# Optimization experiments

Hardware: AMD Instinct MI355X
Metric: run time of the kernel (lower is better)

Reference implementation:

```python
import jax, jax.numpy as jnp
from jax import lax
import numpy as np

HID = 64
NL = 4

def conv2d(x, w, b):
    # x: (N,C,H,W), w: (O,I,kh,kw)
    y = lax.conv_general_dilated(x, w, (1, 1), 'SAME',
                                 dimension_numbers=('NCHW', 'OIHW', 'NCHW'))
    return y + b[None, :, None, None]


def stlstm_cell(x, h, c, m, Wx, bx, Wh, bh, Wm, bm, Wo, bo, Wl, bl):
    # standard PredRNN SpatioTemporalLSTM cell
    xc = conv2d(x, Wx, bx)            # 7*HID channels
    hc = conv2d(h, Wh, bh)            # 4*HID
    mc = conv2d(m, Wm, bm)            # 3*HID
    ix, fx, gx, ixp, fxp, gxp, ox = jnp.split(xc, 7, axis=1)
    ih, fh, gh, oh = jnp.split(hc, 4, axis=1)
    im, fm, gm = jnp.split(mc, 3, axis=1)
    i_t = jax.nn.sigmoid(ix + ih)
    f_t = jax.nn.sigmoid(fx + fh)
    g_t = jnp.tanh(gx + gh)
    c_new = f_t * c + i_t * g_t
    i_tp = jax.nn.sigmoid(ixp + im)
    f_tp = jax.nn.sigmoid(fxp + fm)
    g_tp = jnp.tanh(gxp + gm)
    m_new = f_tp * m + i_tp * g_tp
    mem = jnp.concatenate([c_new, m_new], axis=1)  # 2*HID
    o_t = jax.nn.sigmoid(ox + oh + conv2d(mem, Wo, bo))
    h_new = o_t * jnp.tanh(conv2d(mem, Wl, bl))
    return h_new, c_new, m_new


def setup_inputs() -> dict:
    key = jax.random.key(0)
    ks = jax.random.split(key, 16)
    B, L, C, H, W = 8, 10, 1, 256, 256
    x = jax.random.normal(ks[0], (B, L, C, H, W), dtype=jnp.float32)
    s = 0.02
    d = dict(
        x=x, in_len=10, out_len=10,
        Wx=jax.random.normal(ks[1], (NL, 7 * HID, HID, 3, 3), jnp.float32) * s,
        bx=jnp.zeros((NL, 7 * HID), jnp.float32),
        Wh=jax.random.normal(ks[2], (NL, 4 * HID, HID, 3, 3), jnp.float32) * s,
        bh=jnp.zeros((NL, 4 * HID), jnp.float32),
        Wm=jax.random.normal(ks[3], (NL, 3 * HID, HID, 3, 3), jnp.float32) * s,
        bm=jnp.zeros((NL, 3 * HID), jnp.float32),
        Wo=jax.random.normal(ks[4], (NL, HID, 2 * HID, 3, 3), jnp.float32) * s,
        bo=jnp.zeros((NL, HID), jnp.float32),
        Wl=jax.random.normal(ks[5], (NL, HID, 2 * HID, 1, 1), jnp.float32) * s,
        bl=jnp.zeros((NL, HID), jnp.float32),
        Wd=jax.random.normal(ks[6], (64, HID, 3, 3), jnp.float32) * s,
        bd=jnp.zeros((64,), jnp.float32),
    )
    return d


def reference(x, in_len, out_len, Wx, bx, Wh, bh, Wm, bm, Wo, bo, Wl, bl, Wd, bd):
    B, L, C, H, W = x.shape
    ph, pw = H // 8, W // 8
    # patch_division: space-to-depth 8x8
    xp = x.reshape(B, L, C, 8, ph, 8, pw).transpose(0, 1, 2, 3, 5, 4, 6)
    xp = xp.reshape(B, L, C * 64, ph, pw)
    T = in_len + out_len - 1  # 19 steps
    pad = jnp.zeros((B, T - in_len, C * 64, ph, pw), xp.dtype)
    xs_seq = jnp.moveaxis(jnp.concatenate([xp, pad], axis=1), 1, 0)  # (T,B,64,ph,pw)
    flags = jnp.arange(T) < in_len
    z = jnp.zeros((NL, B, HID, ph, pw), xp.dtype)
    carry0 = (z, z, jnp.zeros((B, HID, ph, pw), xp.dtype),
              jnp.zeros((B, HID, ph, pw), xp.dtype))

    def step(carry, inp):
        hs, cs, m, htop = carry
        xt, flag = inp
        cur = jnp.where(flag, xt, htop)
        new_h, new_c = [], []
        for l in range(NL):
            h, c, m = stlstm_cell(cur, hs[l], cs[l], m,
                                  Wx[l], bx[l], Wh[l], bh[l], Wm[l], bm[l],
                                  Wo[l], bo[l], Wl[l], bl[l])
            new_h.append(h)
            new_c.append(c)
            cur = h
        return (jnp.stack(new_h), jnp.stack(new_c), m, cur), cur

    _, outs = lax.scan(step, carry0, (xs_seq, flags))  # (T,B,HID,ph,pw)
    y = jnp.moveaxis(outs, 0, 1).reshape(B * T, HID, ph, pw)
    y = jax.nn.sigmoid(conv2d(y, Wd, bd)).reshape(B, T, 64, ph, pw)
    # patch_combination: depth-to-space 8x8
    out = y.reshape(B, T, 1, 8, 8, ph, pw).transpose(0, 1, 2, 3, 5, 4, 6)
    out = out.reshape(B, T, 1, 8 * ph, 8 * pw)
    return out
```

## Files before the change

kernel.cpp:

```cpp
#include <hip/hip_runtime.h>
#include <hip/hip_bf16.h>


typedef __bf16 bf16x8 __attribute__((ext_vector_type(8)));
typedef float f32x4 __attribute__((ext_vector_type(4)));

namespace {
constexpr int  T     = 19;
constexpr int  INLEN = 10;

constexpr long OFF_XPB   = 0;
constexpr long OFF_OUTSB = 2621440;
constexpr long OFF_HB    = 7602176;
constexpr long OFF_MB    = 8650752;
constexpr long OFF_C     = 9175040;
constexpr long OFF_M     = 11272192;
constexpr long OFF_MEMB  = 11796480;
constexpr long OFF_OP    = 12320768;
constexpr long OFF_WFA   = 12845056;
constexpr long OFF_WFB   = 13877248;
constexpr long OFF_WFD   = 14041088;
constexpr long OFF_BA    = 14059520;
constexpr long WS_NEEDED_FLOATS = 14061312;
}

__device__ __forceinline__ float sigf(float x)     { return 1.f / (1.f + __expf(-x)); }
__device__ __forceinline__ float tanhfast(float x) { return 2.f / (1.f + __expf(-2.f * x)) - 1.f; }
__device__ __forceinline__ unsigned short f2b(float f) {
  __hip_bfloat16 h = __float2bfloat16(f);
  return __builtin_bit_cast(unsigned short, h);
}
__device__ __forceinline__ f32x4 mfma16(bf16x8 a, bf16x8 b, f32x4 c) {
  return __builtin_amdgcn_mfma_f32_16x16x32_bf16(a, b, c, 0, 0, 0);
}

__global__ __launch_bounds__(448) void kcellA(
    const unsigned short* __restrict__ in0, long in0bs,
    const unsigned short* __restrict__ hB,
    const unsigned short* __restrict__ mBr,
    const unsigned short* __restrict__ wfA,
    const float* __restrict__ bA,
    float* __restrict__ C, float* __restrict__ M,
    unsigned short* __restrict__ mBw,
    unsigned short* __restrict__ memB,
    float* __restrict__ op)
{
  __shared__ __align__(16) char smem[57344];
  unsigned short* sIn = (unsigned short*)smem;
  float* sEx = (float*)smem;

  const int b = blockIdx.x, r0 = blockIdx.y, tid = threadIdx.x;
  const unsigned short* base0 = in0 + (long)b * in0bs;
  const unsigned short* base1 = hB  + (long)b * 65536;
  const unsigned short* base2 = mBr + (long)b * 65536;

  for (int s = tid; s < 3 * 816; s += 448) {
    int inp = s / 816, rem = s - inp * 816;
    int slot = rem >> 3, cg = rem & 7;
    int rr = slot / 34, cl = slot - rr * 34;
    int gr = r0 - 1 + rr, gc = cl - 1;
    const unsigned short* bp = (inp == 0) ? base0 : ((inp == 1) ? base1 : base2);
    uint4 v = make_uint4(0u, 0u, 0u, 0u);
    if ((unsigned)gr < 32u && (unsigned)gc < 32u)
      v = *(const uint4*)(bp + ((long)(gr * 32 + gc) << 6) + cg * 8);
    *(uint4*)(sIn + inp * 6528 + slot * 64 + ((cg ^ (slot & 7)) * 8)) = v;
  }
  __syncthreads();

  const int w = tid >> 6, lane = tid & 63, q = lane >> 4, n16 = lane & 15;
  f32x4 acc[4][2];
  #pragma unroll
  for (int i = 0; i < 4; ++i) { acc[i][0] = (f32x4){0,0,0,0}; acc[i][1] = (f32x4){0,0,0,0}; }

  const unsigned short* sb1 = sIn + ((w < 4) ? 6528 : 13056);
  const unsigned short* wbase = wfA + (long)w * 73728;

  #pragma unroll
  for (int p = 0; p < 2; ++p) {
    const unsigned short* sb = p ? sb1 : sIn;
    #pragma unroll
    for (int tap = 0; tap < 9; ++tap) {
      const int dy = tap / 3, dx = tap - dy * 3;
      #pragma unroll
      for (int cc = 0; cc < 2; ++cc) {
        const unsigned short* wp = wbase + (long)(((p * 9 + tap) * 2 + cc) * 4) * 512 + lane * 8;
        bf16x8 a0 = *(const bf16x8*)(wp);
        bf16x8 a1 = *(const bf16x8*)(wp + 512);
        bf16x8 a2 = *(const bf16x8*)(wp + 1024);
        bf16x8 a3 = *(const bf16x8*)(wp + 1536);
        const int g = cc * 4 + q;
        bf16x8 bf0, bf1;
        { int slot = dy * 34 + n16 + dx;
          bf0 = *(const bf16x8*)(sb + slot * 64 + ((g ^ (slot & 7)) * 8)); }
        { int slot = dy * 34 + 16 + n16 + dx;
          bf1 = *(const bf16x8*)(sb + slot * 64 + ((g ^ (slot & 7)) * 8)); }
        acc[0][0] = mfma16(a0, bf0, acc[0][0]); acc[0][1] = mfma16(a0, bf1, acc[0][1]);
        acc[1][0] = mfma16(a1, bf0, acc[1][0]); acc[1][1] = mfma16(a1, bf1, acc[1][1]);
        acc[2][0] = mfma16(a2, bf0, acc[2][0]); acc[2][1] = mfma16(a2, bf1, acc[2][1]);
        acc[3][0] = mfma16(a3, bf0, acc[3][0]); acc[3][1] = mfma16(a3, bf1, acc[3][1]);
      }
    }
  }

  __syncthreads();
  #pragma unroll
  for (int i = 0; i < 4; ++i)
    #pragma unroll
    for (int j = 0; j < 2; ++j)
      #pragma unroll
      for (int r = 0; r < 4; ++r)
        sEx[w * 2048 + (i * 16 + q * 4 + r) * 32 + (j * 16 + n16)] = acc[i][j][r];
  __syncthreads();

  for (int idx = tid; idx < 2048; idx += 448) {
    const int ch = idx >> 5, pxl = idx & 31;
    const int pxg = r0 * 32 + pxl;
    float iv = sEx[idx]            + bA[ch];
    float fv = sEx[2048 + idx]     + bA[64 + ch];
    float gv = sEx[4096 + idx]     + bA[128 + ch];
    float ov = sEx[6144 + idx]     + bA[192 + ch];
    float i2 = sEx[8192 + idx]     + bA[256 + ch];
    float f2 = sEx[10240 + idx]    + bA[320 + ch];
    float g2 = sEx[12288 + idx]    + bA[384 + ch];
    const long cmo = ((long)b * 64 + ch) * 1024 + pxg;
    float cn = sigf(fv) * C[cmo] + sigf(iv) * tanhfast(gv);
    float mn = sigf(f2) * M[cmo] + sigf(i2) * tanhfast(g2);
    C[cmo] = cn; M[cmo] = mn; op[cmo] = ov;
    const long mo = (long)b * 1024 + pxg;
    memB[mo * 128 + ch]      = f2b(cn);
    memB[mo * 128 + 64 + ch] = f2b(mn);
    mBw[mo * 64 + ch]        = f2b(mn);
  }
}

__global__ __launch_bounds__(512) void kcellB(
    const unsigned short* __restrict__ memB,
    const unsigned short* __restrict__ wfB,
    const float* __restrict__ op, const float* __restrict__ bl,
    unsigned short* __restrict__ hBw, unsigned short* __restrict__ outsBt,
    int writeOuts)
{
  __shared__ __align__(16) char smem[73728];
  unsigned short* sIn = (unsigned short*)smem;
  float* sEx = (float*)smem;

  const int b = blockIdx.x, r0 = blockIdx.y, tid = threadIdx.x;
  const unsigned short* bp = memB + (long)b * 131072;
  for (int s = tid; s < 102 * 16; s += 512) {
    int slot = s >> 4, cg = s & 15;
    int rr = slot / 34, cl = slot - rr * 34;
    int gr = r0 - 1 + rr, gc = cl - 1;
    uint4 v = make_uint4(0u, 0u, 0u, 0u);
    if ((unsigned)gr < 32u && (unsigned)gc < 32u)
      v = *(const uint4*)(bp + ((long)(gr * 32 + gc) << 7) + cg * 8);
    *(uint4*)(sIn + slot * 128 + ((cg ^ (slot & 7)) * 8)) = v;
  }
  __syncthreads();

  const int w = tid >> 6, lane = tid & 63, q = lane >> 4, n16 = lane & 15;
  f32x4 accO[4][2], accL[4][2];
  #pragma unroll
  for (int i = 0; i < 4; ++i) {
    accO[i][0] = (f32x4){0,0,0,0}; accO[i][1] = (f32x4){0,0,0,0};
    accL[i][0] = (f32x4){0,0,0,0}; accL[i][1] = (f32x4){0,0,0,0};
  }

  #pragma unroll
  for (int s5 = 0; s5 < 5; ++s5) {
    const int s = w * 5 + s5;
    const bool isL = (s >= 36);
    const int tap = isL ? 4 : (s >> 2);
    const int cc  = isL ? (s - 36) : (s & 3);
    const int dy = tap / 3, dx = tap - dy * 3;
    const unsigned short* wp = wfB + (long)s * 2048 + lane * 8;
    bf16x8 a0 = *(const bf16x8*)(wp);
    bf16x8 a1 = *(const bf16x8*)(wp + 512);
    bf16x8 a2 = *(const bf16x8*)(wp + 1024);
    bf16x8 a3 = *(const bf16x8*)(wp + 1536);
    const int g = cc * 4 + q;
    bf16x8 bf0, bf1;
    { int slot = dy * 34 + n16 + dx;
      bf0 = *(const bf16x8*)(sIn + slot * 128 + ((g ^ (slot & 7)) * 8)); }
    { int slot = dy * 34 + 16 + n16 + dx;
      bf1 = *(const bf16x8*)(sIn + slot * 128 + ((g ^ (slot & 7)) * 8)); }
    if (isL) {
      accL[0][0] = mfma16(a0, bf0, accL[0][0]); accL[0][1] = mfma16(a0, bf1, accL[0][1]);
      accL[1][0] = mfma16(a1, bf0, accL[1][0]); accL[1][1] = mfma16(a1, bf1, accL[1][1]);
      accL[2][0] = mfma16(a2, bf0, accL[2][0]); accL[2][1] = mfma16(a2, bf1, accL[2][1]);
      accL[3][0] = mfma16(a3, bf0, accL[3][0]); accL[3][1] = mfma16(a3, bf1, accL[3][1]);
    } else {
      accO[0][0] = mfma16(a0, bf0, accO[0][0]); accO[0][1] = mfma16(a0, bf1, accO[0][1]);
      accO[1][0] = mfma16(a1, bf0, accO[1][0]); accO[1][1] = mfma16(a1, bf1, accO[1][1]);
      accO[2][0] = mfma16(a2, bf0, accO[2][0]); accO[2][1] = mfma16(a2, bf1, accO[2][1]);
      accO[3][0] = mfma16(a3, bf0, accO[3][0]); accO[3][1] = mfma16(a3, bf1, accO[3][1]);
    }
  }

  __syncthreads();
  #pragma unroll
  for (int i = 0; i < 4; ++i)
    #pragma unroll
    for (int j = 0; j < 2; ++j)
      #pragma unroll
      for (int r = 0; r < 4; ++r)
        sEx[w * 2048 + (i * 16 + q * 4 + r) * 32 + (j * 16 + n16)] = accO[i][j][r];
  if (w == 7) {
    #pragma unroll
    for (int i = 0; i < 4; ++i)
      #pragma unroll
      for (int j = 0; j < 2; ++j)
        #pragma unroll
        for (int r = 0; r < 4; ++r)
          sEx[16384 + (i * 16 + q * 4 + r) * 32 + (j * 16 + n16)] = accL[i][j][r];
  }
  __syncthreads();

  for (int idx = tid; idx < 2048; idx += 512) {
    const int ch = idx >> 5, pxl = idx & 31;
    const int pxg = r0 * 32 + pxl;
    float o = op[((long)b * 64 + ch) * 1024 + pxg];
    #pragma unroll
    for (int ww = 0; ww < 8; ++ww) o += sEx[ww * 2048 + idx];
    float l = sEx[16384 + idx] + bl[ch];
    unsigned short hv = f2b(sigf(o) * tanhfast(l));
    hBw[((long)b * 1024 + pxg) * 64 + ch] = hv;
    if (writeOuts) outsBt[((long)b * 1024 + pxg) * 64 + ch] = hv;
  }
}

__device__ __forceinline__ void conv3_acc(
    const unsigned short* __restrict__ ip, int ciStride, int ciOff,
    const unsigned short* __restrict__ wf, int ncc, int ccoff,
    unsigned short* sIn, f32x4 (&acc)[4][4])
{
  const int tid = threadIdx.x;
  const int r0  = (int)blockIdx.y * 8;
  for (int s = tid; s < 2720; s += 256) {
    int slot = s >> 3, cg = s & 7;
    int rr = slot / 34, cl = slot - rr * 34;
    int gr = r0 - 1 + rr, gc = cl - 1;
    uint4 v = make_uint4(0u, 0u, 0u, 0u);
    if ((unsigned)gr < 32u && (unsigned)gc < 32u)
      v = *(const uint4*)(ip + (long)(gr * 32 + gc) * ciStride + ciOff + cg * 8);
    *(uint4*)(sIn + slot * 64 + ((cg ^ (slot & 7)) * 8)) = v;
  }
  __syncthreads();
  const int lane = tid & 63, w = tid >> 6;
  const int q = lane >> 4, n16 = lane & 15;
  #pragma unroll
  for (int i = 0; i < 4; ++i)
    #pragma unroll
    for (int j = 0; j < 4; ++j)
      acc[i][j] = (f32x4){0.f, 0.f, 0.f, 0.f};
  #pragma unroll
  for (int tap = 0; tap < 9; ++tap) {
    const int dy = tap / 3, dx = tap - dy * 3;
    #pragma unroll
    for (int cc = 0; cc < 2; ++cc) {
      const unsigned short* wp = wf + (long)(tap * ncc + ccoff + cc) * 2048 + lane * 8;
      bf16x8 a0 = *(const bf16x8*)(wp);
      bf16x8 a1 = *(const bf16x8*)(wp + 512);
      bf16x8 a2 = *(const bf16x8*)(wp + 1024);
      bf16x8 a3 = *(const bf16x8*)(wp + 1536);
      const int cs = cc * 4 + q;
      bf16x8 bfr[4];
      #pragma unroll
      for (int pf = 0; pf < 4; ++pf) {
        int slot = (w * 2 + (pf >> 1) + dy) * 34 + (pf & 1) * 16 + dx + n16;
        bfr[pf] = *(const bf16x8*)(sIn + slot * 64 + ((cs ^ (slot & 7)) * 8));
      }
      #pragma unroll
      for (int j = 0; j < 4; ++j) {
        acc[0][j] = mfma16(a0, bfr[j], acc[0][j]);
        acc[1][j] = mfma16(a1, bfr[j], acc[1][j]);
        acc[2][j] = mfma16(a2, bfr[j], acc[2][j]);
        acc[3][j] = mfma16(a3, bfr[j], acc[3][j]);
      }
    }
  }
}

__global__ __launch_bounds__(256) void kconv_final(
    const unsigned short* __restrict__ outsB,
    const unsigned short* __restrict__ wdf, const float* __restrict__ bd,
    float* __restrict__ dout)
{
  __shared__ __align__(16) unsigned short sIn[21760];
  const int img = blockIdx.x;
  const int b = img / 19, t = img - b * 19;
  f32x4 acc[4][4];
  conv3_acc(outsB + ((long)t * 8 + b) * 65536, 64, 0, wdf, 2, 0, sIn, acc);
  const int tid = threadIdx.x;
  const int lane = tid & 63, w = tid >> 6;
  const int q = lane >> 4, n16 = lane & 15;
  const int r0 = (int)blockIdx.y * 8;
  float* ob = dout + (long)img * 65536;
  #pragma unroll
  for (int i = 0; i < 4; ++i) {
    #pragma unroll
    for (int r = 0; r < 4; ++r) {
      const int co = i * 16 + q * 4 + r;
      const float bv = bd[co];
      #pragma unroll
      for (int j = 0; j < 4; ++j) {
        int row = r0 + w * 2 + (j >> 1);
        int col = (j & 1) * 16 + n16;
        ob[((co >> 3) * 32 + row) * 256 + (co & 7) * 32 + col] = sigf(acc[i][j][r] + bv);
      }
    }
  }
}

__global__ __launch_bounds__(256) void kpatch(const float* __restrict__ x,
                                              unsigned short* __restrict__ xpB)
{
  __shared__ __align__(16) unsigned short sT[2048];
  const int img = blockIdx.x, tid = threadIdx.x;
  const float* xi = x + (long)img * 65536;
  unsigned short* xo = xpB + (long)img * 65536;
  for (int p = 0; p < 32; ++p) {
    __syncthreads();
    int ch = tid >> 2, q0 = (tid & 3) * 8;
    const float* s = xi + ((ch >> 3) * 32 + p) * 256 + (ch & 7) * 32 + q0;
    float4 v0 = *(const float4*)s, v1 = *(const float4*)(s + 4);
    float vv[8] = {v0.x, v0.y, v0.z, v0.w, v1.x, v1.y, v1.z, v1.w};
    #pragma unroll
    for (int k = 0; k < 8; ++k) {
      int qq = q0 + k;
      sT[qq * 64 + (((ch >> 3) ^ (qq & 7)) * 8) + (ch & 7)] = f2b(vv[k]);
    }
    __syncthreads();
    int q = tid >> 3, cg = tid & 7;
    uint4 v = *(const uint4*)(sT + q * 64 + ((cg ^ (q & 7)) * 8));
    *(uint4*)(xo + (long)(p * 32 + q) * 64 + cg * 8) = v;
  }
}

__global__ __launch_bounds__(256) void kprepw(const float* __restrict__ src,
                                              unsigned short* __restrict__ dst,
                                              int Cout, int Cin, int KK)
{
  long n = (long)Cout * Cin * KK;
  long idx = (long)blockIdx.x * 256 + threadIdx.x;
  if (idx >= n) return;
  int ncc = Cin >> 5;
  long tmp = idx >> 3; int e = (int)(idx & 7);
  int lane = (int)(tmp & 63); tmp >>= 6;
  int cf = (int)(tmp & 3); tmp >>= 2;
  int cc = (int)(tmp % ncc); tmp /= ncc;
  int tap = (int)(tmp % KK); int chunk = (int)(tmp / KK);
  int co = chunk * 64 + cf * 16 + (lane & 15);
  int ci = cc * 32 + (lane >> 4) * 8 + e;
  dst[idx] = f2b(src[((long)co * Cin + ci) * KK + tap]);
}

__global__ __launch_bounds__(256) void kpackA(
    const float* __restrict__ Wx, const float* __restrict__ Wh,
    const float* __restrict__ Wm, unsigned short* __restrict__ wfA)
{
  long idx = (long)blockIdx.x * 256 + threadIdx.x;
  if (idx >= 2064384) return;
  int e = (int)(idx & 7);
  long t = idx >> 3;
  int lane = (int)(t & 63); t >>= 6;
  int frag = (int)(t & 3);  t >>= 2;
  int cc   = (int)(t & 1);  t >>= 1;
  int tap  = (int)(t % 9);  t /= 9;
  int p    = (int)(t & 1);  t >>= 1;
  int w    = (int)(t % 7);
  int l    = (int)(t / 7);
  int co = frag * 16 + (lane & 15);
  int ci = cc * 32 + (lane >> 4) * 8 + e;
  const float* src; int row;
  if (w < 4) {
    if (p == 0) { src = Wx + (long)l * 258048; row = (w == 3 ? 384 : w * 64) + co; }
    else        { src = Wh + (long)l * 147456; row = (w == 3 ? 192 : w * 64) + co; }
  } else {
    if (p == 0) { src = Wx + (long)l * 258048; row = 192 + (w - 4) * 64 + co; }
    else        { src = Wm + (long)l * 110592; row = (w - 4) * 64 + co; }
  }
  wfA[idx] = f2b(src[((long)row * 64 + ci) * 9 + tap]);
}

__global__ __launch_bounds__(256) void kpackB(
    const float* __restrict__ Wo, const float* __restrict__ Wl,
    unsigned short* __restrict__ wfB)
{
  long idx = (long)blockIdx.x * 256 + threadIdx.x;
  if (idx >= 327680) return;
  int e = (int)(idx & 7);
  long t = idx >> 3;
  int lane = (int)(t & 63); t >>= 6;
  int frag = (int)(t & 3);  t >>= 2;
  int s    = (int)(t % 40);
  int l    = (int)(t / 40);
  int co = frag * 16 + (lane & 15);
  float v;
  if (s < 36) {
    int tap = s >> 2, cc = s & 3;
    int ci = cc * 32 + (lane >> 4) * 8 + e;
    v = Wo[(long)l * 73728 + ((long)co * 128 + ci) * 9 + tap];
  } else {
    int cc = s - 36;
    int ci = cc * 32 + (lane >> 4) * 8 + e;
    v = Wl[(long)l * 8192 + (long)co * 128 + ci];
  }
  wfB[idx] = f2b(v);
}

__global__ __launch_bounds__(256) void kpackbA(
    const float* __restrict__ bx, const float* __restrict__ bh,
    const float* __restrict__ bm, const float* __restrict__ bo,
    float* __restrict__ bA)
{
  int idx = blockIdx.x * 256 + threadIdx.x;
  if (idx >= 1792) return;
  int ch = idx & 63, w = (idx >> 6) % 7, l = (idx >> 6) / 7;
  const float* bxl = bx + l * 448;
  const float* bhl = bh + l * 256;
  const float* bml = bm + l * 192;
  const float* bol = bo + l * 64;
  float v;
  if (w < 3)       v = bxl[w * 64 + ch] + bhl[w * 64 + ch];
  else if (w == 3) v = bxl[384 + ch] + bhl[192 + ch] + bol[ch];
  else             v = bxl[192 + (w - 4) * 64 + ch] + bml[(w - 4) * 64 + ch];
  bA[idx] = v;
}

extern "C" void kernel_launch(void* const* d_in, const int* in_sizes, int n_in,
                              void* d_out, int out_size, void* d_ws, size_t ws_size,
                              hipStream_t stream)
{
  (void)in_sizes; (void)n_in; (void)out_size;
  if (ws_size < WS_NEEDED_FLOATS * sizeof(float)) return;

  const float* x  = (const float*)d_in[0];
  const float* Wx = (const float*)d_in[3];
  const float* bx = (const float*)d_in[4];
  const float* Wh = (const float*)d_in[5];
  const float* bh = (const float*)d_in[6];
  const float* Wm = (const float*)d_in[7];
  const float* bm = (const float*)d_in[8];
  const float* Wo = (const float*)d_in[9];
  const float* bo = (const float*)d_in[10];
  const float* Wl = (const float*)d_in[11];
  const float* bl = (const float*)d_in[12];
  const float* Wd = (const float*)d_in[13];
  const float* bd = (const float*)d_in[14];
  float* ws  = (float*)d_ws;
  float* out = (float*)d_out;

  unsigned short* xpB   = (unsigned short*)(ws + OFF_XPB);
  unsigned short* outsB = (unsigned short*)(ws + OFF_OUTSB);
  unsigned short* hB    = (unsigned short*)(ws + OFF_HB);
  unsigned short* mB0   = (unsigned short*)(ws + OFF_MB);
  unsigned short* mB1   = mB0 + 524288;
  float*          C     = ws + OFF_C;
  float*          M     = ws + OFF_M;
  unsigned short* memB  = (unsigned short*)(ws + OFF_MEMB);
  float*          OP    = ws + OFF_OP;
  unsigned short* wfA   = (unsigned short*)(ws + OFF_WFA);
  unsigned short* wfB   = (unsigned short*)(ws + OFF_WFB);
  unsigned short* wfD   = (unsigned short*)(ws + OFF_WFD);
  float*          bA    = ws + OFF_BA;

  kpackA<<<dim3(8064), 256, 0, stream>>>(Wx, Wh, Wm, wfA);
  kpackB<<<dim3(1280), 256, 0, stream>>>(Wo, Wl, wfB);
  kpackbA<<<dim3(7), 256, 0, stream>>>(bx, bh, bm, bo, bA);
  kprepw<<<dim3(144), 256, 0, stream>>>(Wd, wfD, 64, 64, 9);
  kpatch<<<dim3(80), 256, 0, stream>>>(x, xpB);
  hipMemsetAsync(ws + OFF_HB, 0, (OFF_MEMB - OFF_HB) * sizeof(float), stream);

  for (int t = 0; t < T; ++t) {
    for (int l = 0; l < 4; ++l) {
      const int cell = t * 4 + l;
      const unsigned short* in0; long ibs;
      if (l == 0) {
        if (t < INLEN) { in0 = xpB + (long)t * 65536; ibs = 655360; }
        else           { in0 = outsB + (long)(t - 1) * 524288; ibs = 65536; }
      } else {
        in0 = hB + (long)(l - 1) * 524288; ibs = 65536;
      }
      const unsigned short* mBr = (cell & 1) ? mB1 : mB0;
      unsigned short*       mBw = (cell & 1) ? mB0 : mB1;
      kcellA<<<dim3(8, 32), 448, 0, stream>>>(
          in0, ibs, hB + (long)l * 524288, mBr,
          wfA + (long)l * 516096, bA + l * 448,
          C + (long)l * 524288, M, mBw, memB, OP);
      kcellB<<<dim3(8, 32), 512, 0, stream>>>(
          memB, wfB + (long)l * 81920, OP, bl + l * 64,
          hB + (long)l * 524288, outsB + (long)t * 524288, (l == 3) ? 1 : 0);
    }
  }
  kconv_final<<<dim3(152, 4), 256, 0, stream>>>(outsB, wfD, bd, out);
}
```

Before: 2.654 ms.

## Restructure ST-LSTM cell kernels so each wave owns output channels across gates

kcellA now tiles two pixel rows per block, with each wave owning a 16-channel group across all seven gates. It reuses weight fragments across rows and applies the gate epilogue straight from registers, without an LDS exchange. kcellB becomes a single wave that computes all 64 output channels for both the 3x3 and 1x1 convs, which removes the cross-wave LDS reduction. Outputs are written as vectorized uint4 stores through a swizzled LDS transpose, and the weight packing kernels are reordered to match. Blocks are much smaller and fewer waves run per block, which raises per-thread register pressure and could reduce occupancy or latency hiding.

```diff
diff --git a/kernel.cpp b/kernel.cpp
--- a/kernel.cpp
+++ b/kernel.cpp
@@ -34,119 +34,140 @@
   return __builtin_amdgcn_mfma_f32_16x16x32_bf16(a, b, c, 0, 0, 0);
 }
 
-__global__ __launch_bounds__(448) void kcellA(
+__device__ __forceinline__ void stage64(const unsigned short* __restrict__ bp,
+                                        unsigned short* dst, int s, int by) {
+  int slot = s >> 3, cg = s & 7;
+  int rr = slot / 34, cl = slot - rr * 34;
+  int gr = by * 2 - 1 + rr, gc = cl - 1;
+  uint4 v = make_uint4(0u, 0u, 0u, 0u);
+  if ((unsigned)gr < 32u && (unsigned)gc < 32u)
+    v = *(const uint4*)(bp + ((long)(gr * 32 + gc) << 6) + cg * 8);
+  *(uint4*)(dst + slot * 64 + ((cg ^ (slot & 7)) * 8)) = v;
+}
+
+template<int NG, int S0, int FOFF>
+__device__ __forceinline__ void conv_section(
+    const unsigned short* sb, const unsigned short* wA,
+    int lane, int q, int n16, f32x4 (&acc)[7][4])
+{
+  #pragma unroll
+  for (int cc = 0; cc < 2; ++cc) {
+    #pragma unroll
+    for (int dx = 0; dx < 3; ++dx) {
+      bf16x8 A[3][NG];
+      #pragma unroll
+      for (int dy = 0; dy < 3; ++dy)
+        #pragma unroll
+        for (int s = 0; s < NG; ++s)
+          A[dy][s] = *(const bf16x8*)(wA +
+              (long)(FOFF + (cc * 3 + dx) * (3 * NG) + dy * NG + s) * 512 + lane * 8);
+      const int cs = cc * 4 + q;
+      #pragma unroll
+      for (int cg = 0; cg < 2; ++cg) {
+        bf16x8 B[4];
+        #pragma unroll
+        for (int ridx = 0; ridx < 4; ++ridx) {
+          const int slot = ridx * 34 + cg * 16 + dx + n16;
+          B[ridx] = *(const bf16x8*)(sb + slot * 64 + ((cs ^ (slot & 7)) * 8));
+        }
+        #pragma unroll
+        for (int s = 0; s < NG; ++s) {
+          acc[S0 + s][cg]     = mfma16(A[0][s], B[0], acc[S0 + s][cg]);
+          acc[S0 + s][cg]     = mfma16(A[1][s], B[1], acc[S0 + s][cg]);
+          acc[S0 + s][cg]     = mfma16(A[2][s], B[2], acc[S0 + s][cg]);
+          acc[S0 + s][2 + cg] = mfma16(A[0][s], B[1], acc[S0 + s][2 + cg]);
+          acc[S0 + s][2 + cg] = mfma16(A[1][s], B[2], acc[S0 + s][2 + cg]);
+          acc[S0 + s][2 + cg] = mfma16(A[2][s], B[3], acc[S0 + s][2 + cg]);
+        }
+      }
+    }
+  }
+}
+
+__global__ __launch_bounds__(128) void kcellA(
     const unsigned short* __restrict__ in0, long in0bs,
     const unsigned short* __restrict__ hB,
     const unsigned short* __restrict__ mBr,
-    const unsigned short* __restrict__ wfA,
-    const float* __restrict__ bA,
+    const unsigned short* __restrict__ wfAl,
+    const float* __restrict__ bAl,
     float* __restrict__ C, float* __restrict__ M,
     unsigned short* __restrict__ mBw,
     unsigned short* __restrict__ memB,
     float* __restrict__ op)
 {
-  __shared__ __align__(16) char smem[57344];
-  unsigned short* sIn = (unsigned short*)smem;
-  float* sEx = (float*)smem;
-
-  const int b = blockIdx.x, r0 = blockIdx.y, tid = threadIdx.x;
-  const unsigned short* base0 = in0 + (long)b * in0bs;
-  const unsigned short* base1 = hB  + (long)b * 65536;
-  const unsigned short* base2 = mBr + (long)b * 65536;
-
-  for (int s = tid; s < 3 * 816; s += 448) {
-    int inp = s / 816, rem = s - inp * 816;
-    int slot = rem >> 3, cg = rem & 7;
-    int rr = slot / 34, cl = slot - rr * 34;
-    int gr = r0 - 1 + rr, gc = cl - 1;
-    const unsigned short* bp = (inp == 0) ? base0 : ((inp == 1) ? base1 : base2);
-    uint4 v = make_uint4(0u, 0u, 0u, 0u);
-    if ((unsigned)gr < 32u && (unsigned)gc < 32u)
-      v = *(const uint4*)(bp + ((long)(gr * 32 + gc) << 6) + cg * 8);
-    *(uint4*)(sIn + inp * 6528 + slot * 64 + ((cg ^ (slot & 7)) * 8)) = v;
-  }
+  __shared__ __align__(16) unsigned short sIn[26112];
+  const int b = blockIdx.x, by = blockIdx.y, z = blockIdx.z, tid = threadIdx.x;
+
+  const unsigned short* p0 = in0 + (long)b * in0bs;
+  const unsigned short* p1 = hB + ((long)b << 16);
+  const unsigned short* p2 = mBr + ((long)b << 16);
+  for (int s = tid; s < 1088; s += 128) stage64(p0, sIn, s, by);
+  for (int s = tid; s < 1088; s += 128) stage64(p1, sIn + 8704, s, by);
+  for (int s = tid; s < 1088; s += 128) stage64(p2, sIn + 17408, s, by);
   __syncthreads();
 
   const int w = tid >> 6, lane = tid & 63, q = lane >> 4, n16 = lane & 15;
-  f32x4 acc[4][2];
-  #pragma unroll
-  for (int i = 0; i < 4; ++i) { acc[i][0] = (f32x4){0,0,0,0}; acc[i][1] = (f32x4){0,0,0,0}; }
-
-  const unsigned short* sb1 = sIn + ((w < 4) ? 6528 : 13056);
-  const unsigned short* wbase = wfA + (long)w * 73728;
-
-  #pragma unroll
-  for (int p = 0; p < 2; ++p) {
-    const unsigned short* sb = p ? sb1 : sIn;
-    #pragma unroll
-    for (int tap = 0; tap < 9; ++tap) {
-      const int dy = tap / 3, dx = tap - dy * 3;
-      #pragma unroll
-      for (int cc = 0; cc < 2; ++cc) {
-        const unsigned short* wp = wbase + (long)(((p * 9 + tap) * 2 + cc) * 4) * 512 + lane * 8;
-        bf16x8 a0 = *(const bf16x8*)(wp);
-        bf16x8 a1 = *(const bf16x8*)(wp + 512);
-        bf16x8 a2 = *(const bf16x8*)(wp + 1024);
-        bf16x8 a3 = *(const bf16x8*)(wp + 1536);
-        const int g = cc * 4 + q;
-        bf16x8 bf0, bf1;
-        { int slot = dy * 34 + n16 + dx;
-          bf0 = *(const bf16x8*)(sb + slot * 64 + ((g ^ (slot & 7)) * 8)); }
-        { int slot = dy * 34 + 16 + n16 + dx;
-          bf1 = *(const bf16x8*)(sb + slot * 64 + ((g ^ (slot & 7)) * 8)); }
-        acc[0][0] = mfma16(a0, bf0, acc[0][0]); acc[0][1] = mfma16(a0, bf1, acc[0][1]);
-        acc[1][0] = mfma16(a1, bf0, acc[1][0]); acc[1][1] = mfma16(a1, bf1, acc[1][1]);
-        acc[2][0] = mfma16(a2, bf0, acc[2][0]); acc[2][1] = mfma16(a2, bf1, acc[2][1]);
-        acc[3][0] = mfma16(a3, bf0, acc[3][0]); acc[3][1] = mfma16(a3, bf1, acc[3][1]);
-      }
-    }
-  }
-
-  __syncthreads();
-  #pragma unroll
-  for (int i = 0; i < 4; ++i)
-    #pragma unroll
-    for (int j = 0; j < 2; ++j)
-      #pragma unroll
-      for (int r = 0; r < 4; ++r)
-        sEx[w * 2048 + (i * 16 + q * 4 + r) * 32 + (j * 16 + n16)] = acc[i][j][r];
-  __syncthreads();
-
-  for (int idx = tid; idx < 2048; idx += 448) {
-    const int ch = idx >> 5, pxl = idx & 31;
-    const int pxg = r0 * 32 + pxl;
-    float iv = sEx[idx]            + bA[ch];
-    float fv = sEx[2048 + idx]     + bA[64 + ch];
-    float gv = sEx[4096 + idx]     + bA[128 + ch];
-    float ov = sEx[6144 + idx]     + bA[192 + ch];
-    float i2 = sEx[8192 + idx]     + bA[256 + ch];
-    float f2 = sEx[10240 + idx]    + bA[320 + ch];
-    float g2 = sEx[12288 + idx]    + bA[384 + ch];
-    const long cmo = ((long)b * 64 + ch) * 1024 + pxg;
-    float cn = sigf(fv) * C[cmo] + sigf(iv) * tanhfast(gv);
-    float mn = sigf(f2) * M[cmo] + sigf(i2) * tanhfast(g2);
-    C[cmo] = cn; M[cmo] = mn; op[cmo] = ov;
-    const long mo = (long)b * 1024 + pxg;
-    memB[mo * 128 + ch]      = f2b(cn);
-    memB[mo * 128 + 64 + ch] = f2b(mn);
-    mBw[mo * 64 + ch]        = f2b(mn);
-  }
-}
-
-__global__ __launch_bounds__(512) void kcellB(
+  const int g = z * 2 + w;
+  const unsigned short* wA = wfAl + (long)g * 129024;
+  f32x4 acc[7][4];
+  #pragma unroll
+  for (int s = 0; s < 7; ++s)
+    #pragma unroll
+    for (int j = 0; j < 4; ++j) acc[s][j] = (f32x4){0.f, 0.f, 0.f, 0.f};
+
+  conv_section<7, 0, 0>  (sIn,         wA, lane, q, n16, acc);
+  conv_section<4, 0, 126>(sIn + 8704,  wA, lane, q, n16, acc);
+  conv_section<3, 4, 198>(sIn + 17408, wA, lane, q, n16, acc);
+  __syncthreads();
+
+  unsigned short* sT = sIn;
+  const int pxr = by * 64;
+  #pragma unroll
+  for (int r = 0; r < 4; ++r) {
+    const int co = g * 16 + q * 4 + r;
+    const float bi  = bAl[co],       bf_ = bAl[64 + co],  bg  = bAl[128 + co];
+    const float bo_ = bAl[192 + co], bi2 = bAl[256 + co], bf2 = bAl[320 + co];
+    const float bg2 = bAl[384 + co];
+    #pragma unroll
+    for (int pf = 0; pf < 4; ++pf) {
+      const int pxl = (pf >> 1) * 32 + (pf & 1) * 16 + n16;
+      const long cmo = ((long)b * 64 + co) * 1024 + pxr + pxl;
+      float cn = sigf(acc[1][pf][r] + bf_) * C[cmo] +
+                 sigf(acc[0][pf][r] + bi)  * tanhfast(acc[2][pf][r] + bg);
+      float mn = sigf(acc[5][pf][r] + bf2) * M[cmo] +
+                 sigf(acc[4][pf][r] + bi2) * tanhfast(acc[6][pf][r] + bg2);
+      C[cmo] = cn; M[cmo] = mn;
+      op[cmo] = acc[3][pf][r] + bo_;
+      const int chc = co & 31;
+      sT[pxl * 64 + (((chc >> 3) ^ (pxl & 7)) * 8) + (chc & 7)] = f2b(cn);
+      const int chm = 32 + chc;
+      sT[pxl * 64 + (((chm >> 3) ^ (pxl & 7)) * 8) + (chm & 7)] = f2b(mn);
+    }
+  }
+  __syncthreads();
+
+  for (int k = 0; k < 4; ++k) {
+    const int u = tid + k * 128;
+    const int pxl = u >> 3, chv = u & 7;
+    uint4 v = *(const uint4*)(sT + pxl * 64 + ((chv ^ (pxl & 7)) * 8));
+    const long pxg = (long)b * 1024 + pxr + pxl;
+    const int chg = (chv < 4) ? (z * 32 + chv * 8) : (64 + z * 32 + (chv - 4) * 8);
+    *(uint4*)(memB + pxg * 128 + chg) = v;
+    if (chv >= 4) *(uint4*)(mBw + pxg * 64 + z * 32 + (chv - 4) * 8) = v;
+  }
+}
+
+__global__ __launch_bounds__(64) void kcellB(
     const unsigned short* __restrict__ memB,
-    const unsigned short* __restrict__ wfB,
+    const unsigned short* __restrict__ wfBl,
     const float* __restrict__ op, const float* __restrict__ bl,
     unsigned short* __restrict__ hBw, unsigned short* __restrict__ outsBt,
     int writeOuts)
 {
-  __shared__ __align__(16) char smem[73728];
-  unsigned short* sIn = (unsigned short*)smem;
-  float* sEx = (float*)smem;
-
+  __shared__ __align__(16) unsigned short sIn[13056];
   const int b = blockIdx.x, r0 = blockIdx.y, tid = threadIdx.x;
-  const unsigned short* bp = memB + (long)b * 131072;
-  for (int s = tid; s < 102 * 16; s += 512) {
+  const unsigned short* bp = memB + ((long)b << 17);
+  for (int s = tid; s < 1632; s += 64) {
     int slot = s >> 4, cg = s & 15;
     int rr = slot / 34, cl = slot - rr * 34;
     int gr = r0 - 1 + rr, gc = cl - 1;
@@ -157,74 +178,80 @@
   }
   __syncthreads();
 
-  const int w = tid >> 6, lane = tid & 63, q = lane >> 4, n16 = lane & 15;
+  const int lane = tid, q = lane >> 4, n16 = lane & 15;
   f32x4 accO[4][2], accL[4][2];
   #pragma unroll
-  for (int i = 0; i < 4; ++i) {
-    accO[i][0] = (f32x4){0,0,0,0}; accO[i][1] = (f32x4){0,0,0,0};
-    accL[i][0] = (f32x4){0,0,0,0}; accL[i][1] = (f32x4){0,0,0,0};
-  }
-
-  #pragma unroll
-  for (int s5 = 0; s5 < 5; ++s5) {
-    const int s = w * 5 + s5;
-    const bool isL = (s >= 36);
-    const int tap = isL ? 4 : (s >> 2);
-    const int cc  = isL ? (s - 36) : (s & 3);
-    const int dy = tap / 3, dx = tap - dy * 3;
-    const unsigned short* wp = wfB + (long)s * 2048 + lane * 8;
-    bf16x8 a0 = *(const bf16x8*)(wp);
-    bf16x8 a1 = *(const bf16x8*)(wp + 512);
-    bf16x8 a2 = *(const bf16x8*)(wp + 1024);
-    bf16x8 a3 = *(const bf16x8*)(wp + 1536);
-    const int g = cc * 4 + q;
-    bf16x8 bf0, bf1;
-    { int slot = dy * 34 + n16 + dx;
-      bf0 = *(const bf16x8*)(sIn + slot * 128 + ((g ^ (slot & 7)) * 8)); }
-    { int slot = dy * 34 + 16 + n16 + dx;
-      bf1 = *(const bf16x8*)(sIn + slot * 128 + ((g ^ (slot & 7)) * 8)); }
-    if (isL) {
-      accL[0][0] = mfma16(a0, bf0, accL[0][0]); accL[0][1] = mfma16(a0, bf1, accL[0][1]);
-      accL[1][0] = mfma16(a1, bf0, accL[1][0]); accL[1][1] = mfma16(a1, bf1, accL[1][1]);
-      accL[2][0] = mfma16(a2, bf0, accL[2][0]); accL[2][1] = mfma16(a2, bf1, accL[2][1]);
-      accL[3][0] = mfma16(a3, bf0, accL[3][0]); accL[3][1] = mfma16(a3, bf1, accL[3][1]);
-    } else {
-      accO[0][0] = mfma16(a0, bf0, accO[0][0]); accO[0][1] = mfma16(a0, bf1, accO[0][1]);
-      accO[1][0] = mfma16(a1, bf0, accO[1][0]); accO[1][1] = mfma16(a1, bf1, accO[1][1]);
-      accO[2][0] = mfma16(a2, bf0, accO[2][0]); accO[2][1] = mfma16(a2, bf1, accO[2][1]);
-      accO[3][0] = mfma16(a3, bf0, accO[3][0]); accO[3][1] = mfma16(a3, bf1, accO[3][1]);
-    }
-  }
-
-  __syncthreads();
-  #pragma unroll
-  for (int i = 0; i < 4; ++i)
-    #pragma unroll
-    for (int j = 0; j < 2; ++j)
-      #pragma unroll
-      for (int r = 0; r < 4; ++r)
-        sEx[w * 2048 + (i * 16 + q * 4 + r) * 32 + (j * 16 + n16)] = accO[i][j][r];
-  if (w == 7) {
-    #pragma unroll
-    for (int i = 0; i < 4; ++i)
-      #pragma unroll
-      for (int j = 0; j < 2; ++j)
+  for (int f = 0; f < 4; ++f) {
+    accO[f][0] = (f32x4){0.f,0.f,0.f,0.f}; accO[f][1] = (f32x4){0.f,0.f,0.f,0.f};
+    accL[f][0] = (f32x4){0.f,0.f,0.f,0.f}; accL[f][1] = (f32x4){0.f,0.f,0.f,0.f};
+  }
+
+  #pragma unroll
+  for (int cc = 0; cc < 4; ++cc) {
+    const int cs = cc * 4 + q;
+    #pragma unroll
+    for (int dx = 0; dx < 3; ++dx) {
+      bf16x8 AO[3][4];
+      #pragma unroll
+      for (int dy = 0; dy < 3; ++dy)
         #pragma unroll
-        for (int r = 0; r < 4; ++r)
-          sEx[16384 + (i * 16 + q * 4 + r) * 32 + (j * 16 + n16)] = accL[i][j][r];
-  }
-  __syncthreads();
-
-  for (int idx = tid; idx < 2048; idx += 512) {
-    const int ch = idx >> 5, pxl = idx & 31;
+        for (int f = 0; f < 4; ++f)
+          AO[dy][f] = *(const bf16x8*)(wfBl +
+              (long)((((cc * 3 + dx) * 3 + dy) * 4) + f) * 512 + lane * 8);
+      #pragma unroll
+      for (int cg = 0; cg < 2; ++cg) {
+        bf16x8 B[3];
+        #pragma unroll
+        for (int dy = 0; dy < 3; ++dy) {
+          const int slot = dy * 34 + cg * 16 + dx + n16;
+          B[dy] = *(const bf16x8*)(sIn + slot * 128 + ((cs ^ (slot & 7)) * 8));
+        }
+        #pragma unroll
+        for (int dy = 0; dy < 3; ++dy)
+          #pragma unroll
+          for (int f = 0; f < 4; ++f)
+            accO[f][cg] = mfma16(AO[dy][f], B[dy], accO[f][cg]);
+      }
+    }
+    bf16x8 AL[4];
+    #pragma unroll
+    for (int f = 0; f < 4; ++f)
+      AL[f] = *(const bf16x8*)(wfBl + (long)(144 + cc * 4 + f) * 512 + lane * 8);
+    #pragma unroll
+    for (int cg = 0; cg < 2; ++cg) {
+      const int slot = 34 + cg * 16 + 1 + n16;
+      bf16x8 Bc = *(const bf16x8*)(sIn + slot * 128 + ((cs ^ (slot & 7)) * 8));
+      #pragma unroll
+      for (int f = 0; f < 4; ++f)
+        accL[f][cg] = mfma16(AL[f], Bc, accL[f][cg]);
+    }
+  }
+  __syncthreads();
+
+  unsigned short* sT = sIn;
+  #pragma unroll
+  for (int pf = 0; pf < 2; ++pf) {
+    const int pxl = pf * 16 + n16;
     const int pxg = r0 * 32 + pxl;
-    float o = op[((long)b * 64 + ch) * 1024 + pxg];
-    #pragma unroll
-    for (int ww = 0; ww < 8; ++ww) o += sEx[ww * 2048 + idx];
-    float l = sEx[16384 + idx] + bl[ch];
-    unsigned short hv = f2b(sigf(o) * tanhfast(l));
-    hBw[((long)b * 1024 + pxg) * 64 + ch] = hv;
-    if (writeOuts) outsBt[((long)b * 1024 + pxg) * 64 + ch] = hv;
+    #pragma unroll
+    for (int f = 0; f < 4; ++f)
+      #pragma unroll
+      for (int r = 0; r < 4; ++r) {
+        const int co = f * 16 + q * 4 + r;
+        float o = accO[f][pf][r] + op[((long)b * 64 + co) * 1024 + pxg];
+        float l = accL[f][pf][r] + bl[co];
+        sT[pxl * 64 + (((co >> 3) ^ (pxl & 7)) * 8) + (co & 7)] =
+            f2b(sigf(o) * tanhfast(l));
+      }
+  }
+  __syncthreads();
+  for (int k = 0; k < 4; ++k) {
+    const int u = tid + k * 64;
+    const int pxl = u >> 3, chv = u & 7;
+    uint4 v = *(const uint4*)(sT + pxl * 64 + ((chv ^ (pxl & 7)) * 8));
+    const long pxg = (long)b * 1024 + r0 * 32 + pxl;
+    *(uint4*)(hBw + pxg * 64 + chv * 8) = v;
+    if (writeOuts) *(uint4*)(outsBt + pxg * 64 + chv * 8) = v;
   }
 }
 
@@ -354,56 +381,63 @@
   dst[idx] = f2b(src[((long)co * Cin + ci) * KK + tap]);
 }
 
-__global__ __launch_bounds__(256) void kpackA(
+__global__ __launch_bounds__(256) void kpackA2(
     const float* __restrict__ Wx, const float* __restrict__ Wh,
     const float* __restrict__ Wm, unsigned short* __restrict__ wfA)
 {
   long idx = (long)blockIdx.x * 256 + threadIdx.x;
   if (idx >= 2064384) return;
   int e = (int)(idx & 7);
-  long t = idx >> 3;
-  int lane = (int)(t & 63); t >>= 6;
-  int frag = (int)(t & 3);  t >>= 2;
-  int cc   = (int)(t & 1);  t >>= 1;
-  int tap  = (int)(t % 9);  t /= 9;
-  int p    = (int)(t & 1);  t >>= 1;
-  int w    = (int)(t % 7);
-  int l    = (int)(t / 7);
-  int co = frag * 16 + (lane & 15);
+  int lane = (int)((idx >> 3) & 63);
+  long f9 = idx >> 9;
+  int frag = (int)(f9 % 252);
+  int g    = (int)((f9 / 252) & 3);
+  int l    = (int)(f9 / 1008);
+  int p, step, dy, s;
+  if (frag < 126)      { p = 0; step = frag / 21; int r2 = frag % 21; dy = r2 / 7; s = r2 % 7; }
+  else if (frag < 198) { p = 1; int f2 = frag - 126; step = f2 / 12; int r2 = f2 % 12; dy = r2 / 4; s = r2 % 4; }
+  else                 { p = 2; int f3 = frag - 198; step = f3 / 9;  int r2 = f3 % 9;  dy = r2 / 3; s = 4 + r2 % 3; }
+  int cc = step / 3, dx = step % 3, tap = dy * 3 + dx;
   int ci = cc * 32 + (lane >> 4) * 8 + e;
-  const float* src; int row;
-  if (w < 4) {
-    if (p == 0) { src = Wx + (long)l * 258048; row = (w == 3 ? 384 : w * 64) + co; }
-    else        { src = Wh + (long)l * 147456; row = (w == 3 ? 192 : w * 64) + co; }
+  int co16 = g * 16 + (lane & 15);
+  float v;
+  if (p == 0) {
+    int rb = (s == 0) ? 0 : (s == 1) ? 64 : (s == 2) ? 128 : (s == 3) ? 384
+           : (s == 4) ? 192 : (s == 5) ? 256 : 320;
+    v = Wx[((long)(l * 448 + rb + co16)) * 576 + ci * 9 + tap];
+  } else if (p == 1) {
+    v = Wh[((long)(l * 256 + s * 64 + co16)) * 576 + ci * 9 + tap];
   } else {
-    if (p == 0) { src = Wx + (long)l * 258048; row = 192 + (w - 4) * 64 + co; }
-    else        { src = Wm + (long)l * 110592; row = (w - 4) * 64 + co; }
-  }
-  wfA[idx] = f2b(src[((long)row * 64 + ci) * 9 + tap]);
-}
-
-__global__ __launch_bounds__(256) void kpackB(
+    v = Wm[((long)(l * 192 + (s - 4) * 64 + co16)) * 576 + ci * 9 + tap];
+  }
+  wfA[idx] = f2b(v);
+}
+
+__global__ __launch_bounds__(256) void kpackB2(
     const float* __restrict__ Wo, const float* __restrict__ Wl,
     unsigned short* __restrict__ wfB)
 {
   long idx = (long)blockIdx.x * 256 + threadIdx.x;
   if (idx >= 327680) return;
   int e = (int)(idx & 7);
-  long t = idx >> 3;
-  int lane = (int)(t & 63); t >>= 6;
-  int frag = (int)(t & 3);  t >>= 2;
-  int s    = (int)(t % 40);
-  int l    = (int)(t / 40);
-  int co = frag * 16 + (lane & 15);
+  int lane = (int)((idx >> 3) & 63);
+  long f9 = idx >> 9;
+  int frag = (int)(f9 % 160);
+  int l    = (int)(f9 / 160);
   float v;
-  if (s < 36) {
-    int tap = s >> 2, cc = s & 3;
+  if (frag < 144) {
+    int t2 = frag >> 2, f = frag & 3;
+    int dy = t2 % 3, sd = t2 / 3;
+    int dx = sd % 3, cc = sd / 3;
+    int co = f * 16 + (lane & 15);
     int ci = cc * 32 + (lane >> 4) * 8 + e;
-    v = Wo[(long)l * 73728 + ((long)co * 128 + ci) * 9 + tap];
+    v = Wo[((long)(l * 64 + co)) * 1152 + ci * 9 + dy * 3 + dx];
   } else {
-    int cc = s - 36;
+    int f2 = frag - 144;
+    int cc = f2 >> 2, f = f2 & 3;
+    int co = f * 16 + (lane & 15);
     int ci = cc * 32 + (lane >> 4) * 8 + e;
-    v = Wl[(long)l * 8192 + (long)co * 128 + ci];
+    v = Wl[((long)(l * 64 + co)) * 128 + ci];
   }
   wfB[idx] = f2b(v);
 }
@@ -464,8 +498,8 @@
   unsigned short* wfD   = (unsigned short*)(ws + OFF_WFD);
   float*          bA    = ws + OFF_BA;
 
-  kpackA<<<dim3(8064), 256, 0, stream>>>(Wx, Wh, Wm, wfA);
-  kpackB<<<dim3(1280), 256, 0, stream>>>(Wo, Wl, wfB);
+  kpackA2<<<dim3(8064), 256, 0, stream>>>(Wx, Wh, Wm, wfA);
+  kpackB2<<<dim3(1280), 256, 0, stream>>>(Wo, Wl, wfB);
   kpackbA<<<dim3(7), 256, 0, stream>>>(bx, bh, bm, bo, bA);
   kprepw<<<dim3(144), 256, 0, stream>>>(Wd, wfD, 64, 64, 9);
   kpatch<<<dim3(80), 256, 0, stream>>>(x, xpB);
@@ -483,11 +517,11 @@
       }
       const unsigned short* mBr = (cell & 1) ? mB1 : mB0;
       unsigned short*       mBw = (cell & 1) ? mB0 : mB1;
-      kcellA<<<dim3(8, 32), 448, 0, stream>>>(
+      kcellA<<<dim3(8, 16, 2), 128, 0, stream>>>(
           in0, ibs, hB + (long)l * 524288, mBr,
           wfA + (long)l * 516096, bA + l * 448,
           C + (long)l * 524288, M, mBw, memB, OP);
-      kcellB<<<dim3(8, 32), 512, 0, stream>>>(
+      kcellB<<<dim3(8, 32), 64, 0, stream>>>(
           memB, wfB + (long)l * 81920, OP, bl + l * 64,
           hB + (long)l * 524288, outsB + (long)t * 524288, (l == 3) ? 1 : 0);
     }
```

Measured after the change: 3.354 ms. 26.4% more time.
